# Kernel tuning notes

Hardware: AMD Instinct MI355X
Metric: run time of the kernel (lower is better)

Reference implementation:

```python
import jax, jax.numpy as jnp
import numpy as np

N = 50000
E = 600000
D = 128


def gcn_conv(x, row, col, w, W, b):
    """PyG GCNConv: add self-loops (weight 1), symmetric deg^-1/2 normalization,
    linear transform, edge-weighted scatter-add aggregation, then bias."""
    n = x.shape[0]
    loop = jnp.arange(n)
    r = jnp.concatenate([row, loop])            # source nodes, [E+N]
    c = jnp.concatenate([col, loop])            # target nodes, [E+N]
    ww = jnp.concatenate([w, jnp.ones((n,), x.dtype)])
    deg = jax.ops.segment_sum(ww, c, num_segments=n)          # weighted in-degree
    dinv = jnp.where(deg > 0, jax.lax.rsqrt(deg), jnp.zeros_like(deg))
    norm = dinv[r] * ww * dinv[c]               # [E+N]
    xl = x @ W                                  # [n, D_out]
    msg = norm[:, None] * xl[r]                 # gather + scale, [E+N, D_out]
    out = jax.ops.segment_sum(msg, c, num_segments=n)
    return out + b


def setup_inputs() -> dict:
    key = jax.random.key(0)
    ks = jax.random.split(key, 12)
    x = jax.random.normal(ks[0], (N, D), dtype=jnp.float32)
    edge_index = jax.random.randint(ks[1], (2, E), 0, N, dtype=jnp.int64)
    edge_weights = jax.random.uniform(ks[2], (E,), dtype=jnp.float32)
    s = 1.0 / np.sqrt(D)
    W1 = jax.random.uniform(ks[3], (D, D), jnp.float32, -s, s)
    b1 = jnp.zeros((D,), jnp.float32)
    W2 = jax.random.uniform(ks[4], (D, D), jnp.float32, -s, s)
    b2 = jnp.zeros((D,), jnp.float32)
    W3 = jax.random.uniform(ks[5], (D, D), jnp.float32, -s, s)
    b3 = jnp.zeros((D,), jnp.float32)
    prelu_w = jnp.array(0.25, jnp.float32)
    return {"x": x, "edge_index": edge_index, "edge_weights": edge_weights,
            "W1": W1, "b1": b1, "W2": W2, "b2": b2, "W3": W3, "b3": b3,
            "prelu_w": prelu_w}


def reference(x, edge_index, edge_weights, W1, b1, W2, b2, W3, b3, prelu_w):
    row, col = edge_index[0], edge_index[1]
    # layer 1: GCNConv -> (dropout: eval, identity) -> ELU
    h = gcn_conv(x, row, col, edge_weights, W1, b1)
    h = jax.nn.elu(h)
    # layer 2: GCNConv -> GELU (torch default = exact erf)
    h = gcn_conv(h, row, col, edge_weights, W2, b2)
    h = jax.nn.gelu(h, approximate=False)
    # layer 3: GCNConv -> PReLU (learnable scalar slope)
    h = gcn_conv(h, row, col, edge_weights, W3, b3)
    h = jnp.where(h >= 0, h, prelu_w * h)
    return h
```

## Files before the change

kernel.cpp:

```cpp
#include <hip/hip_runtime.h>
#include <hip/hip_fp16.h>
#include <math.h>

constexpr int D = 128;

struct __align__(16) H8 { __half2 h[4]; };

typedef _Float16     half8   __attribute__((ext_vector_type(8)));
typedef float        floatx4 __attribute__((ext_vector_type(4)));
typedef unsigned int uint4v  __attribute__((ext_vector_type(4)));
typedef unsigned int uint2v  __attribute__((ext_vector_type(2)));


__device__ __forceinline__ int detect64(const int* __restrict__ ei) {
  int z = 0;
#pragma unroll
  for (int i = 0; i < 8; ++i) z |= ei[2 * i + 1];
  return (z == 0) ? 1 : 0;
}

__device__ __forceinline__ void load_edge(const int* __restrict__ ei, int e, int nE,
                                          int m64, int n, int& r, int& c) {
  if (m64) { r = ei[2 * (size_t)e]; c = ei[2 * ((size_t)nE + e)]; }
  else     { r = ei[(size_t)e];     c = ei[(size_t)nE + e]; }
  r = min(max(r, 0), n - 1);
  c = min(max(c, 0), n - 1);
}

__global__ void k_setup(const float* __restrict__ W1, const float* __restrict__ W2,
                        const float* __restrict__ W3, __half* __restrict__ Wt,
                        unsigned long long* __restrict__ cntdeg, int n) {
  int b = blockIdx.x;
  if (b < 24) {
    int m = b >> 3, s = b & 7;
    const float* W = m == 0 ? W1 : (m == 1 ? W2 : W3);
    __half* o = Wt + (size_t)m * D * D;
    int t = threadIdx.x;
    int nn = t & 127;
    int kh = t >> 7;
    int k0 = s * 16 + kh * 8;
    H8 hv;
#pragma unroll
    for (int jj = 0; jj < 4; ++jj) {
      float f0 = W[(size_t)(k0 + 2 * jj)     * D + nn];
      float f1 = W[(size_t)(k0 + 2 * jj + 1) * D + nn];
      hv.h[jj] = __floats2half2_rn(f0, f1);
    }
    *(H8*)(o + (size_t)nn * D + k0) = hv;
  } else {
    int i = (b - 24) * 256 + threadIdx.x;
    if (i < n) cntdeg[i] = 0ULL;
  }
}

__global__ void k_pos(const int* __restrict__ ei, const float* __restrict__ w,
                      unsigned long long* __restrict__ cntdeg,
                      int2* __restrict__ rc, int* __restrict__ pos, int nE, int n) {
  int e = blockIdx.x * blockDim.x + threadIdx.x;
  if (e >= nE) return;
  int m64 = detect64(ei);
  int r, c;
  load_edge(ei, e, nE, m64, n, r, c);
  rc[e] = make_int2(r, c);
  float wf = fminf(fmaxf(w[e], 0.0f), 65535.0f);
  unsigned long long pk =
      (1ULL << 32) | (unsigned long long)__float2uint_rn(wf * 65536.0f);
  unsigned long long old = atomicAdd(&cntdeg[c], pk);
  pos[e] = (int)(old >> 32);
}

__global__ void k_scan1(const unsigned long long* __restrict__ cntdeg,
                        int* __restrict__ offs, int* __restrict__ bsum, int n) {
  __shared__ int s[256];
  int t = threadIdx.x;
  int i = blockIdx.x * 256 + t;
  int v = 0;
  if (i < n) {
    int cn = (int)(cntdeg[i] >> 32);
    v = (cn + 3) & ~3;
  }
  s[t] = v;
  __syncthreads();
  for (int off = 1; off < 256; off <<= 1) {
    int x = 0;
    if (t >= off) x = s[t - off];
    __syncthreads();
    if (t >= off) s[t] += x;
    __syncthreads();
  }
  if (i < n) offs[i] = s[t] - v;
  if (t == 255) bsum[blockIdx.x] = s[255];
}

__global__ void k_scan2(const int* __restrict__ bsum, int* __restrict__ boff, int nb) {
  __shared__ int s[256];
  int t = threadIdx.x;
  int v = (t < nb) ? bsum[t] : 0;
  s[t] = v;
  __syncthreads();
  for (int off = 1; off < 256; off <<= 1) {
    int x = 0;
    if (t >= off) x = s[t - off];
    __syncthreads();
    if (t >= off) s[t] += x;
    __syncthreads();
  }
  if (t < nb) boff[t] = s[t] - v;
}

__global__ void k_scan3(int* __restrict__ offs, const int* __restrict__ boff,
                        const int* __restrict__ bsum,
                        const unsigned long long* __restrict__ cntdeg,
                        float* __restrict__ dinv, int n, int nb) {
  int i = blockIdx.x * 256 + threadIdx.x;
  if (i < n) {
    offs[i] += boff[blockIdx.x];
    float degf = (float)(unsigned int)(cntdeg[i] & 0xffffffffULL) * (1.0f / 65536.0f);
    dinv[i] = rsqrtf(1.0f + degf);
  }
  if (i == 0) offs[n] = boff[nb - 1] + bsum[nb - 1];
}

__global__ void k_fill(const int2* __restrict__ rc, const int* __restrict__ pos,
                       const float* __restrict__ w, const int* __restrict__ offs,
                       const unsigned long long* __restrict__ cntdeg,
                       const float* __restrict__ dinv,
                       unsigned int* __restrict__ ecf2, int nE, int n) {
  int e = blockIdx.x * blockDim.x + threadIdx.x;
  if (e < nE) {
    int2 p = rc[e];
    int idx = offs[p.y] + pos[e];
    float cf = dinv[p.x] * w[e];
    ecf2[idx] = ((unsigned int)p.x << 16) |
                (unsigned int)__half_as_ushort(__float2half_rn(cf));
  }
  if (e < n) {
    int q0 = offs[e] + (int)(cntdeg[e] >> 32), q1 = offs[e + 1];
    for (int q = q0; q < q1; ++q) ecf2[q] = 0;
  }
}

template <int ACT>
__device__ __forceinline__ float act_f(float x) {
  if (ACT == 1) return x > 0.f ? x : expm1f(x);
  if (ACT == 2) return 0.5f * x * (1.0f + erff(x * 0.70710678118654752440f));
  return x;
}

template <int ACT, typename AT>
__global__ __launch_bounds__(256) void k_gemm(const AT* __restrict__ A,
                                              const __half* __restrict__ Wt,
                                              __half* __restrict__ Y, int n) {
  const int wave = threadIdx.x >> 6;
  const int lane = threadIdx.x & 63;
  const int np = lane & 15;
  const int quad = lane >> 4;
  const int node = blockIdx.x * 64 + wave * 16 + np;
  const int nc = min(node, n - 1);

  half8 b[4];
#pragma unroll
  for (int s = 0; s < 4; ++s) {
    if constexpr (sizeof(AT) == 4) {
      const float* ap = (const float*)A + (size_t)nc * D + s * 32 + quad * 8;
      floatx4 v0 = __builtin_nontemporal_load((const floatx4*)ap);
      floatx4 v1 = __builtin_nontemporal_load((const floatx4*)(ap + 4));
#pragma unroll
      for (int t = 0; t < 4; ++t) {
        b[s][t]     = (_Float16)act_f<ACT>(v0[t]);
        b[s][t + 4] = (_Float16)act_f<ACT>(v1[t]);
      }
    } else {
      half8 raw = __builtin_nontemporal_load(
          (const half8*)((const __half*)A + ((size_t)s * n + nc) * 32 + quad * 8));
#pragma unroll
      for (int t = 0; t < 8; ++t)
        b[s][t] = (_Float16)act_f<ACT>((float)raw[t]);
    }
  }

  floatx4 acc[8];
#pragma unroll
  for (int mt = 0; mt < 8; ++mt) acc[mt] = (floatx4){0.f, 0.f, 0.f, 0.f};

#pragma unroll
  for (int mt = 0; mt < 8; ++mt) {
#pragma unroll
    for (int s = 0; s < 4; ++s) {
      half8 a = *(const half8*)(Wt + (size_t)(mt * 16 + np) * D + s * 32 + quad * 8);
      acc[mt] = __builtin_amdgcn_mfma_f32_16x16x32_f16(a, b[s], acc[mt], 0, 0, 0);
    }
  }

  if (node < n) {
#pragma unroll
    for (int mt = 0; mt < 8; ++mt) {
      __half2 ha = __floats2half2_rn(acc[mt][0], acc[mt][1]);
      __half2 hb = __floats2half2_rn(acc[mt][2], acc[mt][3]);
      uint2v pv;
      pv[0] = *(unsigned int*)&ha;
      pv[1] = *(unsigned int*)&hb;
      int f0 = mt * 16 + quad * 4;
      __builtin_nontemporal_store(
          pv, (uint2v*)(Y + ((size_t)(f0 >> 5) * n + node) * 32 + (f0 & 31)));
    }
  }
}

__device__ __forceinline__ void fmacc8(float* acc, float c, const H8& y) {
  const _Float16* hp = (const _Float16*)&y;
#pragma unroll
  for (int i = 0; i < 8; ++i) acc[i] = fmaf(c, (float)hp[i], acc[i]);
}

__device__ __forceinline__ float cdecode(unsigned int u) {
  return __half2float(__ushort_as_half((unsigned short)(u & 0xffffu)));
}

__device__ __forceinline__ void gather4(H8* y, uint4v u, const __half* __restrict__ Yc,
                                        int j) {
#pragma unroll
  for (int i = 0; i < 4; ++i)
    y[i] = *(const H8*)(Yc + (size_t)(u[i] >> 16) * 32 + j * 8);
}

__device__ __forceinline__ void accum4(float* acc, uint4v u, const H8* y) {
#pragma unroll
  for (int i = 0; i < 4; ++i) fmacc8(acc, cdecode(u[i]), y[i]);
}

template <int PRELU, typename OutT>
__global__ __launch_bounds__(256) void k_agg(const __half* __restrict__ Y,
                                             const int* __restrict__ offs,
                                             const unsigned int* __restrict__ ecf2,
                                             const float* __restrict__ dinv,
                                             const float* __restrict__ bias,
                                             const float* __restrict__ pw,
                                             OutT* __restrict__ OUT, int n) {
  const int chunk = blockIdx.x & 3;
  const int t = threadIdx.x;
  const int node = (blockIdx.x >> 2) * 32 + (t >> 3);
  const int sub = (t >> 2) & 1;
  const int j = t & 3;
  if (node >= n) return;
  const __half* Yc = Y + (size_t)chunk * n * 32;
  float dc = dinv[node];
  float acc[8] = {0.f, 0.f, 0.f, 0.f, 0.f, 0.f, 0.f, 0.f};

  H8 ys{};
  if (sub == 0) ys = *(const H8*)(Yc + (size_t)node * 32 + j * 8);

  int lo = offs[node], hi = offs[node + 1];
  int nb4 = (hi - lo) >> 2;
  int em = lo + (((nb4 + 1) >> 1) << 2);
  int b0 = sub ? em : lo;
  int be = sub ? hi : em;

  for (int b = b0; b < be; b += 8) {
    bool has2 = (be - b) > 4;
    uint4v u0 = __builtin_nontemporal_load((const uint4v*)(ecf2 + b));
    uint4v u1{};
    if (has2) u1 = __builtin_nontemporal_load((const uint4v*)(ecf2 + b + 4));
    H8 y0[4], y1[4];
    gather4(y0, u0, Yc, j);
    if (has2) gather4(y1, u1, Yc, j);
    accum4(acc, u0, y0);
    if (has2) accum4(acc, u1, y1);
  }
  if (sub == 0) fmacc8(acc, dc, ys);

  floatx4 b4 = *(const floatx4*)(bias + chunk * 32 + j * 8 + sub * 4);
  float o[4];
#pragma unroll
  for (int i = 0; i < 4; ++i) {
    float mine  = sub ? acc[4 + i] : acc[i];
    float other = sub ? acc[i]     : acc[4 + i];
    float recv = __shfl_xor(other, 4, 64);
    o[i] = dc * (mine + recv) + b4[i];
  }
  if (PRELU) {
    float wv = *pw;
#pragma unroll
    for (int i = 0; i < 4; ++i) o[i] = o[i] >= 0.f ? o[i] : wv * o[i];
  }
  if constexpr (sizeof(OutT) == 4) {
    floatx4 ov = {o[0], o[1], o[2], o[3]};
    __builtin_nontemporal_store(
        ov, (floatx4*)((float*)OUT + (size_t)node * D + chunk * 32 + j * 8 + sub * 4));
  } else {
    __half2 ha = __floats2half2_rn(o[0], o[1]);
    __half2 hb = __floats2half2_rn(o[2], o[3]);
    uint2v pv;
    pv[0] = *(unsigned int*)&ha;
    pv[1] = *(unsigned int*)&hb;
    __builtin_nontemporal_store(
        pv, (uint2v*)((__half*)OUT + ((size_t)chunk * n + node) * 32 + j * 8 + sub * 4));
  }
}

extern "C" void kernel_launch(void* const* d_in, const int* in_sizes, int n_in,
                              void* d_out, int out_size, void* d_ws, size_t ws_size,
                              hipStream_t stream) {
  const float* x  = (const float*)d_in[0];
  const int*   ei = (const int*)d_in[1];
  const float* w  = (const float*)d_in[2];
  const float* W1 = (const float*)d_in[3];
  const float* b1 = (const float*)d_in[4];
  const float* W2 = (const float*)d_in[5];
  const float* b2 = (const float*)d_in[6];
  const float* W3 = (const float*)d_in[7];
  const float* b3 = (const float*)d_in[8];
  const float* pw = (const float*)d_in[9];
  const int N = in_sizes[0] / D;
  const int E = in_sizes[2];
  float* out = (float*)d_out;

  char* wsb = (char*)d_ws;
  size_t off = 0;
  auto alloc = [&](size_t bytes) {
    void* p = wsb + off;
    off = (off + bytes + 255) & ~(size_t)255;
    return p;
  };
  float*              dinv   = (float*)alloc((size_t)N * 4);
  unsigned long long* cntdeg = (unsigned long long*)alloc((size_t)N * 8);
  int*                offs   = (int*)alloc((size_t)(N + 1) * 4);
  int*                bsum   = (int*)alloc(256 * 4);
  int*                boff   = (int*)alloc(256 * 4);
  unsigned int*       ecf2   = (unsigned int*)alloc(((size_t)E + 3 * (size_t)N + 64) * 4);
  __half*             Wt     = (__half*)alloc((size_t)3 * D * D * 2);
  __half*             Y      = (__half*)alloc((size_t)N * D * 2);
  __half*             h      = (__half*)alloc((size_t)N * D * 2);
  int2*               rc     = (int2*)Y;
  int*                pos    = (int*)((char*)Y + (size_t)E * 8);

  const int nbN = (N + 255) / 256;
  const int eb  = (E + 255) / 256;
  const int fb  = ((E > N ? E : N) + 255) / 256;

  hipLaunchKernelGGL(k_setup, dim3(24 + nbN), dim3(256), 0, stream, W1, W2, W3, Wt, cntdeg, N);
  hipLaunchKernelGGL(k_pos,   dim3(eb),  dim3(256), 0, stream, ei, w, cntdeg, rc, pos, E, N);
  hipLaunchKernelGGL(k_scan1, dim3(nbN), dim3(256), 0, stream, cntdeg, offs, bsum, N);
  hipLaunchKernelGGL(k_scan2, dim3(1),   dim3(256), 0, stream, bsum, boff, nbN);
  hipLaunchKernelGGL(k_scan3, dim3(nbN), dim3(256), 0, stream, offs, boff, bsum, cntdeg, dinv, N, nbN);
  hipLaunchKernelGGL(k_fill,  dim3(fb),  dim3(256), 0, stream, rc, pos, w, offs, cntdeg, dinv, ecf2, E, N);

  const int gb = (N + 63) / 64;
  const int ab = 4 * ((N + 31) / 32);

  hipLaunchKernelGGL((k_gemm<0, float>),  dim3(gb), dim3(256), 0, stream, x, Wt,             Y, N);
  hipLaunchKernelGGL((k_agg<0, __half>),  dim3(ab), dim3(256), 0, stream, Y, offs, ecf2, dinv, b1, pw, h, N);
  hipLaunchKernelGGL((k_gemm<1, __half>), dim3(gb), dim3(256), 0, stream, h, Wt + D * D,     Y, N);
  hipLaunchKernelGGL((k_agg<0, __half>),  dim3(ab), dim3(256), 0, stream, Y, offs, ecf2, dinv, b2, pw, h, N);
  hipLaunchKernelGGL((k_gemm<2, __half>), dim3(gb), dim3(256), 0, stream, h, Wt + 2 * D * D, Y, N);
  hipLaunchKernelGGL((k_agg<1, float>),   dim3(ab), dim3(256), 0, stream, Y, offs, ecf2, dinv, b3, pw, out, N);
}
```

Before: 309.0 us.

## Fuse first GEMM with edge counting, pad degree counters, stage edges in LDS

Merges the layer-1 GEMM and the edge position/degree atomic kernel into one launch so the two independent tasks share the GPU. rc/pos move from aliasing Y into their own buffers to allow this. Each per-node degree counter is padded to 64 bytes to reduce atomic contention on shared cache lines. The aggregation kernel now preloads each block's edge-coefficient segment into shared memory, up to a capacity limit, before gathering. This costs more workspace, extra zeroing work and a block-wide barrier.

Result: faster. 289.3 us (-6.4%).

```diff
diff --git a/kernel.cpp b/kernel.cpp
--- a/kernel.cpp
+++ b/kernel.cpp
@@ -3,6 +3,7 @@
 #include <math.h>
 
 constexpr int D = 128;
+constexpr int CAP = 2048;
 
 struct __align__(16) H8 { __half2 h[4]; };
 
@@ -29,7 +30,7 @@
 
 __global__ void k_setup(const float* __restrict__ W1, const float* __restrict__ W2,
                         const float* __restrict__ W3, __half* __restrict__ Wt,
-                        unsigned long long* __restrict__ cntdeg, int n) {
+                        unsigned long long* __restrict__ cntdeg, int n8) {
   int b = blockIdx.x;
   if (b < 24) {
     int m = b >> 3, s = b & 7;
@@ -49,14 +50,99 @@
     *(H8*)(o + (size_t)nn * D + k0) = hv;
   } else {
     int i = (b - 24) * 256 + threadIdx.x;
-    if (i < n) cntdeg[i] = 0ULL;
-  }
-}
-
-__global__ void k_pos(const int* __restrict__ ei, const float* __restrict__ w,
-                      unsigned long long* __restrict__ cntdeg,
-                      int2* __restrict__ rc, int* __restrict__ pos, int nE, int n) {
-  int e = blockIdx.x * blockDim.x + threadIdx.x;
+    if (i < n8) cntdeg[i] = 0ULL;
+  }
+}
+
+template <int ACT>
+__device__ __forceinline__ float act_f(float x) {
+  if (ACT == 1) return x > 0.f ? x : expm1f(x);
+  if (ACT == 2) return 0.5f * x * (1.0f + erff(x * 0.70710678118654752440f));
+  return x;
+}
+
+template <int ACT, typename AT>
+__device__ __forceinline__ void gemm_body(int bid, const AT* __restrict__ A,
+                                          const __half* __restrict__ Wt,
+                                          __half* __restrict__ Y, int n) {
+  const int wave = threadIdx.x >> 6;
+  const int lane = threadIdx.x & 63;
+  const int np = lane & 15;
+  const int quad = lane >> 4;
+  const int node = bid * 64 + wave * 16 + np;
+  const int nc = min(node, n - 1);
+
+  half8 b[4];
+#pragma unroll
+  for (int s = 0; s < 4; ++s) {
+    if constexpr (sizeof(AT) == 4) {
+      const float* ap = (const float*)A + (size_t)nc * D + s * 32 + quad * 8;
+      floatx4 v0 = __builtin_nontemporal_load((const floatx4*)ap);
+      floatx4 v1 = __builtin_nontemporal_load((const floatx4*)(ap + 4));
+#pragma unroll
+      for (int t = 0; t < 4; ++t) {
+        b[s][t]     = (_Float16)act_f<ACT>(v0[t]);
+        b[s][t + 4] = (_Float16)act_f<ACT>(v1[t]);
+      }
+    } else {
+      half8 raw = __builtin_nontemporal_load(
+          (const half8*)((const __half*)A + ((size_t)s * n + nc) * 32 + quad * 8));
+#pragma unroll
+      for (int t = 0; t < 8; ++t)
+        b[s][t] = (_Float16)act_f<ACT>((float)raw[t]);
+    }
+  }
+
+  floatx4 acc[8];
+#pragma unroll
+  for (int mt = 0; mt < 8; ++mt) acc[mt] = (floatx4){0.f, 0.f, 0.f, 0.f};
+
+#pragma unroll
+  for (int mt = 0; mt < 8; ++mt) {
+#pragma unroll
+    for (int s = 0; s < 4; ++s) {
+      half8 a = *(const half8*)(Wt + (size_t)(mt * 16 + np) * D + s * 32 + quad * 8);
+      acc[mt] = __builtin_amdgcn_mfma_f32_16x16x32_f16(a, b[s], acc[mt], 0, 0, 0);
+    }
+  }
+
+  if (node < n) {
+#pragma unroll
+    for (int mt = 0; mt < 8; ++mt) {
+      __half2 ha = __floats2half2_rn(acc[mt][0], acc[mt][1]);
+      __half2 hb = __floats2half2_rn(acc[mt][2], acc[mt][3]);
+      uint2v pv;
+      pv[0] = *(unsigned int*)&ha;
+      pv[1] = *(unsigned int*)&hb;
+      int f0 = mt * 16 + quad * 4;
+      __builtin_nontemporal_store(
+          pv, (uint2v*)(Y + ((size_t)(f0 >> 5) * n + node) * 32 + (f0 & 31)));
+    }
+  }
+}
+
+template <int ACT, typename AT>
+__global__ __launch_bounds__(256) void k_gemm(const AT* __restrict__ A,
+                                              const __half* __restrict__ Wt,
+                                              __half* __restrict__ Y, int n) {
+  gemm_body<ACT, AT>(blockIdx.x, A, Wt, Y, n);
+}
+
+__global__ __launch_bounds__(256) void k_posgemm(const float* __restrict__ x,
+                                                 const __half* __restrict__ Wt,
+                                                 __half* __restrict__ Y,
+                                                 const int* __restrict__ ei,
+                                                 const float* __restrict__ w,
+                                                 unsigned long long* __restrict__ cntdeg,
+                                                 int2* __restrict__ rc,
+                                                 int* __restrict__ pos,
+                                                 int nE, int n, int gb) {
+  int b = blockIdx.x;
+  if (b < gb) {
+    gemm_body<0, float>(b, x, Wt, Y, n);
+    return;
+  }
+  int e = (b - gb) * blockDim.x + threadIdx.x;
   if (e >= nE) return;
   int m64 = detect64(ei);
   int r, c;
@@ -65,7 +151,7 @@
   float wf = fminf(fmaxf(w[e], 0.0f), 65535.0f);
   unsigned long long pk =
       (1ULL << 32) | (unsigned long long)__float2uint_rn(wf * 65536.0f);
-  unsigned long long old = atomicAdd(&cntdeg[c], pk);
+  unsigned long long old = atomicAdd(&cntdeg[(size_t)c << 3], pk);
   pos[e] = (int)(old >> 32);
 }
 
@@ -76,7 +162,7 @@
   int i = blockIdx.x * 256 + t;
   int v = 0;
   if (i < n) {
-    int cn = (int)(cntdeg[i] >> 32);
+    int cn = (int)(cntdeg[(size_t)i << 3] >> 32);
     v = (cn + 3) & ~3;
   }
   s[t] = v;
@@ -115,7 +201,8 @@
   int i = blockIdx.x * 256 + threadIdx.x;
   if (i < n) {
     offs[i] += boff[blockIdx.x];
-    float degf = (float)(unsigned int)(cntdeg[i] & 0xffffffffULL) * (1.0f / 65536.0f);
+    float degf =
+        (float)(unsigned int)(cntdeg[(size_t)i << 3] & 0xffffffffULL) * (1.0f / 65536.0f);
     dinv[i] = rsqrtf(1.0f + degf);
   }
   if (i == 0) offs[n] = boff[nb - 1] + bsum[nb - 1];
@@ -135,75 +222,8 @@
                 (unsigned int)__half_as_ushort(__float2half_rn(cf));
   }
   if (e < n) {
-    int q0 = offs[e] + (int)(cntdeg[e] >> 32), q1 = offs[e + 1];
+    int q0 = offs[e] + (int)(cntdeg[(size_t)e << 3] >> 32), q1 = offs[e + 1];
     for (int q = q0; q < q1; ++q) ecf2[q] = 0;
-  }
-}
-
-template <int ACT>
-__device__ __forceinline__ float act_f(float x) {
-  if (ACT == 1) return x > 0.f ? x : expm1f(x);
-  if (ACT == 2) return 0.5f * x * (1.0f + erff(x * 0.70710678118654752440f));
-  return x;
-}
-
-template <int ACT, typename AT>
-__global__ __launch_bounds__(256) void k_gemm(const AT* __restrict__ A,
-                                              const __half* __restrict__ Wt,
-                                              __half* __restrict__ Y, int n) {
-  const int wave = threadIdx.x >> 6;
-  const int lane = threadIdx.x & 63;
-  const int np = lane & 15;
-  const int quad = lane >> 4;
-  const int node = blockIdx.x * 64 + wave * 16 + np;
-  const int nc = min(node, n - 1);
-
-  half8 b[4];
-#pragma unroll
-  for (int s = 0; s < 4; ++s) {
-    if constexpr (sizeof(AT) == 4) {
-      const float* ap = (const float*)A + (size_t)nc * D + s * 32 + quad * 8;
-      floatx4 v0 = __builtin_nontemporal_load((const floatx4*)ap);
-      floatx4 v1 = __builtin_nontemporal_load((const floatx4*)(ap + 4));
-#pragma unroll
-      for (int t = 0; t < 4; ++t) {
-        b[s][t]     = (_Float16)act_f<ACT>(v0[t]);
-        b[s][t + 4] = (_Float16)act_f<ACT>(v1[t]);
-      }
-    } else {
-      half8 raw = __builtin_nontemporal_load(
-          (const half8*)((const __half*)A + ((size_t)s * n + nc) * 32 + quad * 8));
-#pragma unroll
-      for (int t = 0; t < 8; ++t)
-        b[s][t] = (_Float16)act_f<ACT>((float)raw[t]);
-    }
-  }
-
-  floatx4 acc[8];
-#pragma unroll
-  for (int mt = 0; mt < 8; ++mt) acc[mt] = (floatx4){0.f, 0.f, 0.f, 0.f};
-
-#pragma unroll
-  for (int mt = 0; mt < 8; ++mt) {
-#pragma unroll
-    for (int s = 0; s < 4; ++s) {
-      half8 a = *(const half8*)(Wt + (size_t)(mt * 16 + np) * D + s * 32 + quad * 8);
-      acc[mt] = __builtin_amdgcn_mfma_f32_16x16x32_f16(a, b[s], acc[mt], 0, 0, 0);
-    }
-  }
-
-  if (node < n) {
-#pragma unroll
-    for (int mt = 0; mt < 8; ++mt) {
-      __half2 ha = __floats2half2_rn(acc[mt][0], acc[mt][1]);
-      __half2 hb = __floats2half2_rn(acc[mt][2], acc[mt][3]);
-      uint2v pv;
-      pv[0] = *(unsigned int*)&ha;
-      pv[1] = *(unsigned int*)&hb;
-      int f0 = mt * 16 + quad * 4;
-      __builtin_nontemporal_store(
-          pv, (uint2v*)(Y + ((size_t)(f0 >> 5) * n + node) * 32 + (f0 & 31)));
-    }
   }
 }
 
@@ -237,11 +257,23 @@
                                              const float* __restrict__ bias,
                                              const float* __restrict__ pw,
                                              OutT* __restrict__ OUT, int n) {
+  __shared__ unsigned int sc[CAP];
   const int chunk = blockIdx.x & 3;
   const int t = threadIdx.x;
-  const int node = (blockIdx.x >> 2) * 32 + (t >> 3);
+  const int node0 = (blockIdx.x >> 2) * 32;
+  const int node = node0 + (t >> 3);
   const int sub = (t >> 2) & 1;
   const int j = t & 3;
+
+  const int seg_lo = offs[node0];
+  const int seg_hi = offs[min(node0 + 32, n)];
+  const int segN = min(seg_hi - seg_lo, CAP);
+  for (int i = t * 4; i < segN; i += 1024) {
+    uint4v v = __builtin_nontemporal_load((const uint4v*)(ecf2 + seg_lo + i));
+    *(uint4v*)&sc[i] = v;
+  }
+  __syncthreads();
+
   if (node >= n) return;
   const __half* Yc = Y + (size_t)chunk * n * 32;
   float dc = dinv[node];
@@ -258,9 +290,15 @@
 
   for (int b = b0; b < be; b += 8) {
     bool has2 = (be - b) > 4;
-    uint4v u0 = __builtin_nontemporal_load((const uint4v*)(ecf2 + b));
+    int k0 = b - seg_lo;
+    uint4v u0 = (k0 < CAP) ? *(const uint4v*)&sc[k0]
+                           : *(const uint4v*)(ecf2 + b);
     uint4v u1{};
-    if (has2) u1 = __builtin_nontemporal_load((const uint4v*)(ecf2 + b + 4));
+    if (has2) {
+      int k1 = k0 + 4;
+      u1 = (k1 < CAP) ? *(const uint4v*)&sc[k1]
+                      : *(const uint4v*)(ecf2 + b + 4);
+    }
     H8 y0[4], y1[4];
     gather4(y0, u0, Yc, j);
     if (has2) gather4(y1, u1, Yc, j);
@@ -323,7 +361,7 @@
     return p;
   };
   float*              dinv   = (float*)alloc((size_t)N * 4);
-  unsigned long long* cntdeg = (unsigned long long*)alloc((size_t)N * 8);
+  unsigned long long* cntdeg = (unsigned long long*)alloc((size_t)N * 64);
   int*                offs   = (int*)alloc((size_t)(N + 1) * 4);
   int*                bsum   = (int*)alloc(256 * 4);
   int*                boff   = (int*)alloc(256 * 4);
@@ -331,24 +369,25 @@
   __half*             Wt     = (__half*)alloc((size_t)3 * D * D * 2);
   __half*             Y      = (__half*)alloc((size_t)N * D * 2);
   __half*             h      = (__half*)alloc((size_t)N * D * 2);
-  int2*               rc     = (int2*)Y;
-  int*                pos    = (int*)((char*)Y + (size_t)E * 8);
+  int2*               rc     = (int2*)alloc((size_t)E * 8);
+  int*                pos    = (int*)alloc((size_t)E * 4);
 
   const int nbN = (N + 255) / 256;
   const int eb  = (E + 255) / 256;
   const int fb  = ((E > N ? E : N) + 255) / 256;
-
-  hipLaunchKernelGGL(k_setup, dim3(24 + nbN), dim3(256), 0, stream, W1, W2, W3, Wt, cntdeg, N);
-  hipLaunchKernelGGL(k_pos,   dim3(eb),  dim3(256), 0, stream, ei, w, cntdeg, rc, pos, E, N);
-  hipLaunchKernelGGL(k_scan1, dim3(nbN), dim3(256), 0, stream, cntdeg, offs, bsum, N);
-  hipLaunchKernelGGL(k_scan2, dim3(1),   dim3(256), 0, stream, bsum, boff, nbN);
-  hipLaunchKernelGGL(k_scan3, dim3(nbN), dim3(256), 0, stream, offs, boff, bsum, cntdeg, dinv, N, nbN);
-  hipLaunchKernelGGL(k_fill,  dim3(fb),  dim3(256), 0, stream, rc, pos, w, offs, cntdeg, dinv, ecf2, E, N);
-
-  const int gb = (N + 63) / 64;
-  const int ab = 4 * ((N + 31) / 32);
-
-  hipLaunchKernelGGL((k_gemm<0, float>),  dim3(gb), dim3(256), 0, stream, x, Wt,             Y, N);
+  const int n8  = N * 8;
+  const int zb  = (n8 + 255) / 256;
+  const int gb  = (N + 63) / 64;
+  const int ab  = 4 * ((N + 31) / 32);
+
+  hipLaunchKernelGGL(k_setup,   dim3(24 + zb), dim3(256), 0, stream, W1, W2, W3, Wt, cntdeg, n8);
+  hipLaunchKernelGGL(k_posgemm, dim3(gb + eb), dim3(256), 0, stream, x, Wt, Y, ei, w, cntdeg,
+                     rc, pos, E, N, gb);
+  hipLaunchKernelGGL(k_scan1,   dim3(nbN), dim3(256), 0, stream, cntdeg, offs, bsum, N);
+  hipLaunchKernelGGL(k_scan2,   dim3(1),   dim3(256), 0, stream, bsum, boff, nbN);
+  hipLaunchKernelGGL(k_scan3,   dim3(nbN), dim3(256), 0, stream, offs, boff, bsum, cntdeg, dinv, N, nbN);
+  hipLaunchKernelGGL(k_fill,    dim3(fb),  dim3(256), 0, stream, rc, pos, w, offs, cntdeg, dinv, ecf2, E, N);
+
   hipLaunchKernelGGL((k_agg<0, __half>),  dim3(ab), dim3(256), 0, stream, Y, offs, ecf2, dinv, b1, pw, h, N);
   hipLaunchKernelGGL((k_gemm<1, __half>), dim3(gb), dim3(256), 0, stream, h, Wt + D * D,     Y, N);
   hipLaunchKernelGGL((k_agg<0, __half>),  dim3(ab), dim3(256), 0, stream, Y, offs, ecf2, dinv, b2, pw, h, N);
```
